# Kernel optimization log

Hardware: AMD Instinct MI355X
Metric: run time of the kernel (lower is better)

## Reference

```python
import jax, jax.numpy as jnp
import numpy as np

B, FEAT, FIELD, K = 16384, 2048, 32, 64

def setup_inputs() -> dict:
    key = jax.random.key(0)
    k1, k2, k3, k4 = jax.random.split(key, 4)
    x = jax.random.normal(k1, (B, FEAT), dtype=jnp.float32)
    # nn.Linear(feature_size, 1): weight [1, FEAT] (use vector), bias [1] (scalar)
    w = jax.random.normal(k2, (FEAT,), dtype=jnp.float32) / np.sqrt(FEAT)
    b = jax.random.normal(k3, (), dtype=jnp.float32)
    # v ~ N(0, 0.01) as in torch.normal(0, 0.01, ...)
    v = 0.01 * jax.random.normal(k4, (FEAT, FIELD, K), dtype=jnp.float32)
    return {"x": x, "w": w, "b": b, "v": v}

def reference(x, w, b, v):
    # linear part: Linear(feature_size, 1).squeeze() -> [B]
    linear_part = x @ w + b  # [B]
    # field_x = tensordot(x, v, dims=1) -> [B, FIELD, K]
    field_x = jnp.einsum('bf,fsk->bsk', x, v)
    # sum_{i<j} sum_k f_i * f_j  ==  0.5 * (||sum_i f_i||^2 - sum_i ||f_i||^2)
    s = field_x.sum(axis=1)                      # [B, K]
    sq = (field_x * field_x).sum(axis=(1, 2))    # [B]
    interaction = 0.5 * ((s * s).sum(axis=-1) - sq)  # [B]
    return jax.nn.sigmoid(linear_part + interaction)
```

## Files before the change

### kernel.cpp

```cpp
#include <hip/hip_runtime.h>
#include <cstdint>
#include <cstddef>

#define B_ROWS 16384
#define FEAT   2048
#define FIELD  32
#define KDIM   64
#define NCOLS  2048
#define NAUG   2176

using half8   = __attribute__((ext_vector_type(8))) _Float16;
using half4   = __attribute__((ext_vector_type(4))) _Float16;
using floatx4 = __attribute__((ext_vector_type(4))) float;

__device__ __forceinline__ void load_lds16(const void* g, void* l) {
  __builtin_amdgcn_global_load_lds((const __attribute__((address_space(1))) void*)g,
                                   (__attribute__((address_space(3))) void*)l, 16, 0, 0);
}

__global__ __launch_bounds__(256) void k_prep(const float* __restrict__ x,
                                              const float* __restrict__ v,
                                              const float* __restrict__ w,
                                              _Float16* __restrict__ xh,
                                              _Float16* __restrict__ vt,
                                              float* __restrict__ arg) {
  const int bb = blockIdx.x;
  const int t = threadIdx.x;
  if (bb < 8192) {
    size_t i = ((size_t)bb * 256 + t) * 16;
    float4 v0 = *(const float4*)(x + i);
    float4 v1 = *(const float4*)(x + i + 4);
    float4 v2 = *(const float4*)(x + i + 8);
    float4 v3 = *(const float4*)(x + i + 12);
    half8 h0 = { (_Float16)v0.x, (_Float16)v0.y, (_Float16)v0.z, (_Float16)v0.w,
                 (_Float16)v1.x, (_Float16)v1.y, (_Float16)v1.z, (_Float16)v1.w };
    half8 h1 = { (_Float16)v2.x, (_Float16)v2.y, (_Float16)v2.z, (_Float16)v2.w,
                 (_Float16)v3.x, (_Float16)v3.y, (_Float16)v3.z, (_Float16)v3.w };
    *(half8*)(xh + i) = h0;
    *(half8*)(xh + i + 8) = h1;
  } else if (bb < 9216) {
    __shared__ _Float16 tile[64 * 68];
    const int b2 = bb - 8192;
    const int f0 = (b2 >> 5) * 64;
    const int n0 = (b2 & 31) * 64;
#pragma unroll
    for (int j = 0; j < 4; ++j) {
      int c = j * 256 + t;
      int row = c >> 4;
      int col = (c & 15) * 4;
      float4 val = *(const float4*)(v + (size_t)(f0 + row) * NCOLS + n0 + col);
      tile[row * 68 + col + 0] = (_Float16)val.x;
      tile[row * 68 + col + 1] = (_Float16)val.y;
      tile[row * 68 + col + 2] = (_Float16)val.z;
      tile[row * 68 + col + 3] = (_Float16)val.w;
    }
    __syncthreads();
#pragma unroll
    for (int j = 0; j < 4; ++j) {
      int c = j * 256 + t;
      int nl = c >> 4;
      int fl = (c & 15) * 4;
      half4 h = { tile[(fl + 0) * 68 + nl], tile[(fl + 1) * 68 + nl],
                  tile[(fl + 2) * 68 + nl], tile[(fl + 3) * 68 + nl] };
      *(half4*)(vt + (size_t)(n0 + nl) * FEAT + f0 + fl) = h;
    }
  } else if (bb < 9728) {
    const int k = t & 63;
    const int f = (bb - 9216) * 4 + (t >> 6);
    float s = 0.f;
#pragma unroll
    for (int si = 0; si < FIELD; ++si) s += v[(size_t)f * NCOLS + si * KDIM + k];
    vt[(size_t)(NCOLS + k) * FEAT + f] = (_Float16)s;
  } else if (bb < 10240) {
    int idx = (bb - 9728) * 256 + t;
    int r = NCOLS + KDIM + (idx >> 11);
    int f = idx & 2047;
    vt[(size_t)r * FEAT + f] = (r == NCOLS + KDIM) ? (_Float16)w[f] : (_Float16)0.f;
  } else {
    arg[(bb - 10240) * 256 + t] = 0.f;
  }
}

__global__ __launch_bounds__(256) void k_gemm(const _Float16* __restrict__ xh,
                                              const _Float16* __restrict__ vt,
                                              float* __restrict__ arg) {
  __shared__ __align__(16) _Float16 lds_a[128 * 64];
  __shared__ __align__(16) _Float16 lds_b[128 * 64];
  const int t = threadIdx.x;
  const int m0 = blockIdx.x * 128;
  const int n0 = blockIdx.y * 128;
  const int lane = t & 63;
  const int wave = t >> 6;
  const int wm = (wave & 1) * 64;
  const int wn = (wave >> 1) * 64;
  const int lr = lane & 15;
  const int lk = (lane >> 4) * 8;

  floatx4 acc[4][4] = {};

  for (int k0 = 0; k0 < FEAT; k0 += 64) {
#pragma unroll
    for (int i = 0; i < 4; ++i) {
      int c = i * 256 + t;
      int row = c >> 3;
      int g = (c & 7) ^ (row & 7);
      load_lds16(xh + (size_t)(m0 + row) * FEAT + k0 + g * 8, lds_a + c * 8);
      load_lds16(vt + (size_t)(n0 + row) * FEAT + k0 + g * 8, lds_b + c * 8);
    }
    __syncthreads();
#pragma unroll
    for (int ks = 0; ks < 64; ks += 32) {
      const int kc = (ks + lk) >> 3;
      half8 af[4], bf[4];
#pragma unroll
      for (int f = 0; f < 4; ++f) {
        int ma = wm + f * 16 + lr;
        int nb = wn + f * 16 + lr;
        af[f] = *(const half8*)(lds_a + ma * 64 + (kc ^ (ma & 7)) * 8);
        bf[f] = *(const half8*)(lds_b + nb * 64 + (kc ^ (nb & 7)) * 8);
      }
#pragma unroll
      for (int fm = 0; fm < 4; ++fm)
#pragma unroll
        for (int fn = 0; fn < 4; ++fn)
          acc[fm][fn] = __builtin_amdgcn_mfma_f32_16x16x32_f16(af[fm], bf[fn],
                                                               acc[fm][fn], 0, 0, 0);
    }
    __syncthreads();
  }

  const int cq = lane >> 4;
#pragma unroll
  for (int fm = 0; fm < 4; ++fm) {
#pragma unroll
    for (int r = 0; r < 4; ++r) {
      float contrib = 0.f;
#pragma unroll
      for (int fn = 0; fn < 4; ++fn) {
        int col = n0 + wn + fn * 16 + lr;
        float vv = acc[fm][fn][r];
        float q = vv * vv;
        if (col < NCOLS)                contrib -= 0.5f * q;
        else if (col < NCOLS + KDIM)    contrib += 0.5f * q;
        else if (col == NCOLS + KDIM)   contrib += vv;
      }
      contrib += __shfl_xor(contrib, 1);
      contrib += __shfl_xor(contrib, 2);
      contrib += __shfl_xor(contrib, 4);
      contrib += __shfl_xor(contrib, 8);
      if (lr == 0) atomicAdd(&arg[m0 + wm + fm * 16 + cq * 4 + r], contrib);
    }
  }
}

__global__ __launch_bounds__(256) void k_fin(const float* __restrict__ arg,
                                             const float* __restrict__ b,
                                             float* __restrict__ out) {
  int i = blockIdx.x * 256 + threadIdx.x;
  float z = arg[i] + b[0];
  out[i] = 1.f / (1.f + __expf(-z));
}

extern "C" void kernel_launch(void* const* d_in, const int* in_sizes, int n_in,
                              void* d_out, int out_size, void* d_ws, size_t ws_size,
                              hipStream_t stream) {
  const float* x = (const float*)d_in[0];
  const float* w = (const float*)d_in[1];
  const float* b = (const float*)d_in[2];
  const float* v = (const float*)d_in[3];
  float* out = (float*)d_out;

  char* ws = (char*)d_ws;
  _Float16* xh  = (_Float16*)ws;
  _Float16* vt  = (_Float16*)(ws + 67108864);
  float*    arg = (float*)(ws + 67108864 + 8912896);

  k_prep<<<10304, 256, 0, stream>>>(x, v, w, xh, vt, arg);
  k_gemm<<<dim3(128, 17), 256, 0, stream>>>(xh, vt, arg);
  k_fin<<<64, 256, 0, stream>>>(arg, b, out);
}
```

Measured before the change: 409.6 us.

## Double-buffer LDS tiles and switch GEMM to 32x32x16 MFMA

```diff
diff --git a/kernel.cpp b/kernel.cpp
--- a/kernel.cpp
+++ b/kernel.cpp
@@ -9,9 +9,9 @@
 #define NCOLS  2048
 #define NAUG   2176
 
-using half8   = __attribute__((ext_vector_type(8))) _Float16;
-using half4   = __attribute__((ext_vector_type(4))) _Float16;
-using floatx4 = __attribute__((ext_vector_type(4))) float;
+using half8    = __attribute__((ext_vector_type(8))) _Float16;
+using half4    = __attribute__((ext_vector_type(4))) _Float16;
+using floatx16 = __attribute__((ext_vector_type(16))) float;
 
 __device__ __forceinline__ void load_lds16(const void* g, void* l) {
   __builtin_amdgcn_global_load_lds((const __attribute__((address_space(1))) void*)g,
@@ -84,8 +84,8 @@
 __global__ __launch_bounds__(256) void k_gemm(const _Float16* __restrict__ xh,
                                               const _Float16* __restrict__ vt,
                                               float* __restrict__ arg) {
-  __shared__ __align__(16) _Float16 lds_a[128 * 64];
-  __shared__ __align__(16) _Float16 lds_b[128 * 64];
+  __shared__ __align__(16) _Float16 lds_a[2][128 * 64];
+  __shared__ __align__(16) _Float16 lds_b[2][128 * 64];
   const int t = threadIdx.x;
   const int m0 = blockIdx.x * 128;
   const int n0 = blockIdx.y * 128;
@@ -93,51 +93,57 @@
   const int wave = t >> 6;
   const int wm = (wave & 1) * 64;
   const int wn = (wave >> 1) * 64;
-  const int lr = lane & 15;
-  const int lk = (lane >> 4) * 8;
+  const int lr = lane & 31;
+  const int lh = lane >> 5;
 
-  floatx4 acc[4][4] = {};
+  floatx16 acc[2][2] = {};
 
-  for (int k0 = 0; k0 < FEAT; k0 += 64) {
+  auto stage = [&](int buf, int k0) {
 #pragma unroll
     for (int i = 0; i < 4; ++i) {
       int c = i * 256 + t;
       int row = c >> 3;
       int g = (c & 7) ^ (row & 7);
-      load_lds16(xh + (size_t)(m0 + row) * FEAT + k0 + g * 8, lds_a + c * 8);
-      load_lds16(vt + (size_t)(n0 + row) * FEAT + k0 + g * 8, lds_b + c * 8);
+      load_lds16(xh + (size_t)(m0 + row) * FEAT + k0 + g * 8, &lds_a[buf][c * 8]);
+      load_lds16(vt + (size_t)(n0 + row) * FEAT + k0 + g * 8, &lds_b[buf][c * 8]);
     }
-    __syncthreads();
+  };
+
+  stage(0, 0);
+  __syncthreads();
+
+  for (int it = 0; it < 32; ++it) {
+    const int cur = it & 1;
+    if (it + 1 < 32) stage(cur ^ 1, (it + 1) * 64);
 #pragma unroll
-    for (int ks = 0; ks < 64; ks += 32) {
-      const int kc = (ks + lk) >> 3;
-      half8 af[4], bf[4];
+    for (int ks = 0; ks < 4; ++ks) {
+      const int kc = ks * 2 + lh;
+      half8 af[2], bf[2];
 #pragma unroll
-      for (int f = 0; f < 4; ++f) {
-        int ma = wm + f * 16 + lr;
-        int nb = wn + f * 16 + lr;
-        af[f] = *(const half8*)(lds_a + ma * 64 + (kc ^ (ma & 7)) * 8);
-        bf[f] = *(const half8*)(lds_b + nb * 64 + (kc ^ (nb & 7)) * 8);
+      for (int f = 0; f < 2; ++f) {
+        int ma = wm + f * 32 + lr;
+        int nb = wn + f * 32 + lr;
+        af[f] = *(const half8*)(&lds_a[cur][ma * 64 + (kc ^ (ma & 7)) * 8]);
+        bf[f] = *(const half8*)(&lds_b[cur][nb * 64 + (kc ^ (nb & 7)) * 8]);
       }
 #pragma unroll
-      for (int fm = 0; fm < 4; ++fm)
+      for (int fm = 0; fm < 2; ++fm)
 #pragma unroll
-        for (int fn = 0; fn < 4; ++fn)
-          acc[fm][fn] = __builtin_amdgcn_mfma_f32_16x16x32_f16(af[fm], bf[fn],
+        for (int fn = 0; fn < 2; ++fn)
+          acc[fm][fn] = __builtin_amdgcn_mfma_f32_32x32x16_f16(af[fm], bf[fn],
                                                                acc[fm][fn], 0, 0, 0);
     }
     __syncthreads();
   }
 
-  const int cq = lane >> 4;
 #pragma unroll
-  for (int fm = 0; fm < 4; ++fm) {
+  for (int fm = 0; fm < 2; ++fm) {
 #pragma unroll
-    for (int r = 0; r < 4; ++r) {
+    for (int r = 0; r < 16; ++r) {
       float contrib = 0.f;
 #pragma unroll
-      for (int fn = 0; fn < 4; ++fn) {
-        int col = n0 + wn + fn * 16 + lr;
+      for (int fn = 0; fn < 2; ++fn) {
+        int col = n0 + wn + fn * 32 + lr;
         float vv = acc[fm][fn][r];
         float q = vv * vv;
         if (col < NCOLS)                contrib -= 0.5f * q;
@@ -148,7 +154,11 @@
       contrib += __shfl_xor(contrib, 2);
       contrib += __shfl_xor(contrib, 4);
       contrib += __shfl_xor(contrib, 8);
-      if (lr == 0) atomicAdd(&arg[m0 + wm + fm * 16 + cq * 4 + r], contrib);
+      contrib += __shfl_xor(contrib, 16);
+      if (lr == 0) {
+        int m = m0 + wm + fm * 32 + (r & 3) + 8 * (r >> 2) + 4 * lh;
+        atomicAdd(&arg[m], contrib);
+      }
     }
   }
 }
```

Measured after the change: 426.2 us. 1.04x slower.

## Pre-pack B into MFMA fragment layout and double-buffer A tiles in LDS

Applied to the files above, without the earlier changes.

```diff
diff --git a/kernel.cpp b/kernel.cpp
--- a/kernel.cpp
+++ b/kernel.cpp
@@ -81,49 +81,87 @@
   }
 }
 
+__global__ __launch_bounds__(256) void k_packb(const _Float16* __restrict__ vt,
+                                               _Float16* __restrict__ vt_p) {
+  const int nblk = blockIdx.x;
+  const int k0 = blockIdx.y;
+  const int t = threadIdx.x;
+  _Float16* base = vt_p + ((size_t)nblk * 32 + k0) * 8192;
+#pragma unroll
+  for (int i = 0; i < 4; ++i) {
+    int oc = i * 256 + t;
+    int lane = oc & 63;
+    int g = (oc >> 6) & 7;
+    int ks = oc >> 9;
+    int n = nblk * 128 + g * 16 + (lane & 15);
+    int f8 = k0 * 64 + ks * 32 + (lane >> 4) * 8;
+    half8 h = *(const half8*)(vt + (size_t)n * FEAT + f8);
+    *(half8*)(base + oc * 8) = h;
+  }
+}
+
 __global__ __launch_bounds__(256) void k_gemm(const _Float16* __restrict__ xh,
-                                              const _Float16* __restrict__ vt,
+                                              const _Float16* __restrict__ vt_p,
                                               float* __restrict__ arg) {
-  __shared__ __align__(16) _Float16 lds_a[128 * 64];
-  __shared__ __align__(16) _Float16 lds_b[128 * 64];
+  __shared__ __align__(16) _Float16 lds_a[2][128 * 64];
   const int t = threadIdx.x;
   const int m0 = blockIdx.x * 128;
-  const int n0 = blockIdx.y * 128;
+  const int nblk = blockIdx.y;
   const int lane = t & 63;
   const int wave = t >> 6;
-  const int wm = (wave & 1) * 64;
-  const int wn = (wave >> 1) * 64;
+  const int wmb = wave & 1;
+  const int wnb = wave >> 1;
+  const int wm = wmb * 64;
   const int lr = lane & 15;
-  const int lk = (lane >> 4) * 8;
-
-  floatx4 acc[4][4] = {};
-
-  for (int k0 = 0; k0 < FEAT; k0 += 64) {
+
+  const _Float16* bbase = vt_p + (size_t)nblk * 32 * 8192;
+
+  auto stageA = [&](int buf, int k0h) {
 #pragma unroll
     for (int i = 0; i < 4; ++i) {
       int c = i * 256 + t;
       int row = c >> 3;
       int g = (c & 7) ^ (row & 7);
-      load_lds16(xh + (size_t)(m0 + row) * FEAT + k0 + g * 8, lds_a + c * 8);
-      load_lds16(vt + (size_t)(n0 + row) * FEAT + k0 + g * 8, lds_b + c * 8);
-    }
-    __syncthreads();
-#pragma unroll
-    for (int ks = 0; ks < 64; ks += 32) {
-      const int kc = (ks + lk) >> 3;
-      half8 af[4], bf[4];
+      load_lds16(xh + (size_t)(m0 + row) * FEAT + k0h + g * 8, &lds_a[buf][c * 8]);
+    }
+  };
+
+  half8 bf[2][2][4];
+  auto loadB = [&](int buf, int k0i) {
+#pragma unroll
+    for (int ks = 0; ks < 2; ++ks)
+#pragma unroll
+      for (int fn = 0; fn < 4; ++fn)
+        bf[buf][ks][fn] = *(const half8*)(bbase +
+            ((size_t)((k0i * 2 + ks) * 8 + wnb * 4 + fn) * 64 + lane) * 8);
+  };
+
+  floatx4 acc[4][4] = {};
+
+  stageA(0, 0);
+  loadB(0, 0);
+  __syncthreads();
+
+  for (int it = 0; it < 32; ++it) {
+    const int cur = it & 1;
+    if (it + 1 < 32) {
+      stageA(cur ^ 1, (it + 1) * 64);
+      loadB(cur ^ 1, it + 1);
+    }
+#pragma unroll
+    for (int ks = 0; ks < 2; ++ks) {
+      const int kc = ks * 4 + (lane >> 4);
+      half8 af[4];
 #pragma unroll
       for (int f = 0; f < 4; ++f) {
         int ma = wm + f * 16 + lr;
-        int nb = wn + f * 16 + lr;
-        af[f] = *(const half8*)(lds_a + ma * 64 + (kc ^ (ma & 7)) * 8);
-        bf[f] = *(const half8*)(lds_b + nb * 64 + (kc ^ (nb & 7)) * 8);
+        af[f] = *(const half8*)(&lds_a[cur][ma * 64 + (kc ^ (ma & 7)) * 8]);
       }
 #pragma unroll
       for (int fm = 0; fm < 4; ++fm)
 #pragma unroll
         for (int fn = 0; fn < 4; ++fn)
-          acc[fm][fn] = __builtin_amdgcn_mfma_f32_16x16x32_f16(af[fm], bf[fn],
+          acc[fm][fn] = __builtin_amdgcn_mfma_f32_16x16x32_f16(af[fm], bf[cur][ks][fn],
                                                                acc[fm][fn], 0, 0, 0);
     }
     __syncthreads();
@@ -137,7 +175,7 @@
       float contrib = 0.f;
 #pragma unroll
       for (int fn = 0; fn < 4; ++fn) {
-        int col = n0 + wn + fn * 16 + lr;
+        int col = nblk * 128 + wnb * 64 + fn * 16 + lr;
         float vv = acc[fm][fn][r];
         float q = vv * vv;
         if (col < NCOLS)                contrib -= 0.5f * q;
@@ -171,11 +209,13 @@
   float* out = (float*)d_out;
 
   char* ws = (char*)d_ws;
-  _Float16* xh  = (_Float16*)ws;
-  _Float16* vt  = (_Float16*)(ws + 67108864);
-  float*    arg = (float*)(ws + 67108864 + 8912896);
+  _Float16* xh   = (_Float16*)ws;
+  _Float16* vt   = (_Float16*)(ws + 67108864);
+  _Float16* vt_p = (_Float16*)(ws + 67108864 + 8912896);
+  float*    arg  = (float*)(ws + 67108864 + 2 * 8912896);
 
   k_prep<<<10304, 256, 0, stream>>>(x, v, w, xh, vt, arg);
-  k_gemm<<<dim3(128, 17), 256, 0, stream>>>(xh, vt, arg);
+  k_packb<<<dim3(17, 32), 256, 0, stream>>>(vt, vt_p);
+  k_gemm<<<dim3(128, 17), 256, 0, stream>>>(xh, vt_p, arg);
   k_fin<<<64, 256, 0, stream>>>(arg, b, out);
 }
```

Measured after the change: 1.013 ms. 2.47x slower.
